# Kernel tuning notes

Hardware: AMD Instinct MI355X
Metric: run time of the kernel (lower is better)

Reference implementation:

```python
import jax, jax.numpy as jnp
import numpy as np
import math

B, S, HID, H = 1, 2048, 1024, 16
D = HID // H  # head_dim = 64


def setup_inputs() -> dict:
    key = jax.random.key(0)
    ks = jax.random.split(key, 12)
    s = 0.02
    x = jax.random.normal(ks[0], (B, S, HID), jnp.float32)
    Wq = jax.random.normal(ks[1], (HID, HID), jnp.float32) * s
    bq = jnp.zeros((HID,), jnp.float32)
    Wk = jax.random.normal(ks[2], (HID, HID), jnp.float32) * s
    bk = jnp.zeros((HID,), jnp.float32)
    Wv = jax.random.normal(ks[3], (HID, HID), jnp.float32) * s
    bv = jnp.zeros((HID,), jnp.float32)
    Wo = jax.random.normal(ks[4], (HID, HID), jnp.float32) * s
    bo = jnp.zeros((HID,), jnp.float32)
    # nn.Parameter(torch.ones(3,3)) at init; small noise so the bias is non-degenerate
    cmw = jnp.ones((3, 3), jnp.float32) + 0.1 * jax.random.normal(ks[5], (3, 3), jnp.float32)
    # full causal [B,S,S] mask so the mask.shape[1]==seq_len branch is taken
    mask = jnp.tril(jnp.ones((B, S, S), jnp.int32))
    modality_info = jax.random.randint(ks[6], (B, S), 0, 3, dtype=jnp.int64)
    return dict(x=x, Wq=Wq, bq=bq, Wk=Wk, bk=bk, Wv=Wv, bv=bv, Wo=Wo, bo=bo,
                cmw=cmw, mask=mask, modality_info=modality_info)


def reference(x, Wq, bq, Wk, bk, Wv, bv, Wo, bo, cmw, mask, modality_info):
    b, s, _ = x.shape
    # QKV projections (torch Linear: y = x @ W.T + b), split into heads [B,H,S,D]
    q = (x @ Wq.T + bq).reshape(b, s, H, D).transpose(0, 2, 1, 3)
    k = (x @ Wk.T + bk).reshape(b, s, H, D).transpose(0, 2, 1, 3)
    v = (x @ Wv.T + bv).reshape(b, s, H, D).transpose(0, 2, 1, 3)
    scores = jnp.einsum('bhqd,bhkd->bhqk', q, k) / math.sqrt(D)  # [B,H,S,S]
    # cross-modal bias: gather from 3x3 table via pairwise modality indices -> [B,S,S]
    bias = cmw[modality_info[:, :, None], modality_info[:, None, :]]
    scores = scores + bias[:, None, :, :]  # equals original broadcast when B==1
    scores = jnp.where(mask[:, None, :, :] == 0, -1e9, scores)
    attn = jax.nn.softmax(scores, axis=-1)  # dropout is identity in eval
    ctx = jnp.einsum('bhqk,bhkd->bhqd', attn, v)          # [B,H,S,D]
    ctx = ctx.transpose(0, 2, 1, 3).reshape(b, s, HID)    # [B,S,HID]
    return ctx @ Wo.T + bo
```

## Files before the change

kernel.cpp:

```cpp
#include <hip/hip_runtime.h>
#include <hip/hip_bf16.h>
#include <math.h>

#define S_LEN 2048
#define HID   1024
#define NHEAD 16

using bf16x8 = __attribute__((ext_vector_type(8))) short;
using bf16x4 = __attribute__((ext_vector_type(4))) short;
using f32x4  = __attribute__((ext_vector_type(4))) float;

__device__ __forceinline__ float bf2f(short s) {
  union { unsigned u; float f; } c;
  c.u = ((unsigned)(unsigned short)s) << 16;
  return c.f;
}
__device__ __forceinline__ short f2bf(float f) {
  union { float f; unsigned u; } c; c.f = f;
  unsigned u = c.u;
  unsigned r = (u + 0x7fffu + ((u >> 16) & 1u)) >> 16;
  return (short)r;
}
__device__ __forceinline__ float loadf(const void* base, long idx, int is_bf) {
  return is_bf ? bf2f(((const short*)base)[idx]) : ((const float*)base)[idx];
}
__device__ __forceinline__ void gl_lds16(const void* g, void* l) {
  __builtin_amdgcn_global_load_lds(
      (const __attribute__((address_space(1))) void*)g,
      (__attribute__((address_space(3))) void*)l, 16, 0, 0);
}

__global__ __launch_bounds__(256) void convert5(
    const void* __restrict__ s0, const void* __restrict__ s1, const void* __restrict__ s2,
    const void* __restrict__ s3, const void* __restrict__ s4,
    short* __restrict__ d0, short* __restrict__ d1, short* __restrict__ d2,
    short* __restrict__ d3, short* __restrict__ d4,
    const int* __restrict__ modw, int* __restrict__ flags) {
  __shared__ int sh_isbf;
  const int t = threadIdx.x;

  if (t < 64) {
    const unsigned* xw = (const unsigned*)s0;
    int cnt = 0;
    for (int i = t; i < 1024; i += 64) {
      const unsigned fld = (xw[i] >> 7) & 0xFFu;
      cnt += (fld >= 100u && fld <= 135u) ? 1 : 0;
    }
    for (int m = 1; m < 64; m <<= 1) cnt += __shfl_xor(cnt, m);
    if (t == 0) sh_isbf = (cnt >= 512) ? 1 : 0;
  }
  __syncthreads();
  const int is_bf = sh_isbf;

  if (blockIdx.x == 0 && blockIdx.y == 0 && t < 64) {
    int odd = 0;
    for (int i = 0; i < 4; ++i) {
      const int wv = modw[2 * (t + 64 * i) + 1];
      odd += (wv != 0) ? 1 : 0;
    }
    for (int m = 1; m < 64; m <<= 1) odd += __shfl_xor(odd, m);
    if (t == 0) {
      flags[0] = is_bf;
      flags[1] = (odd == 0) ? 1 : 0;
    }
  }

  const int a = blockIdx.y;
  const void* src = (a == 0) ? s0 : (a == 1) ? s1 : (a == 2) ? s2 : (a == 3) ? s3 : s4;
  short* dst = (a == 0) ? d0 : (a == 1) ? d1 : (a == 2) ? d2 : (a == 3) ? d3 : d4;
  const long n = (a == 0) ? (2L << 20) : (1L << 20);
  long i = (long)(blockIdx.x * 256 + t) * 8;
  const long stride = (long)gridDim.x * 256 * 8;
  if (is_bf) {
    for (; i < n; i += stride)
      *(bf16x8*)(dst + i) = *(const bf16x8*)((const short*)src + i);
  } else {
    for (; i < n; i += stride) {
      const float* p = (const float*)src + i;
      bf16x8 r;
#pragma unroll
      for (int j = 0; j < 8; ++j) r[j] = f2bf(p[j]);
      *(bf16x8*)(dst + i) = r;
    }
  }
}

template <int BM, int BN>
__global__ __launch_bounds__(256) void gemm_bt3(
    const short* __restrict__ A,
    const short* __restrict__ W0, const short* __restrict__ W1, const short* __restrict__ W2,
    const void* __restrict__ b0, const void* __restrict__ b1, const void* __restrict__ b2,
    void* __restrict__ C0, void* __restrict__ C1, void* __restrict__ C2,
    const int* __restrict__ flags, int nbn, int store_f32)
{
  constexpr int K = 1024;
  constexpr int N = 1024;
  constexpr int WM = (BM == 128) ? 2 : 1;
  constexpr int WN = 4 / WM;
  constexpr int MI = (BM / 16) / WM;
  constexpr int NI = (BN / 16) / WN;
  __shared__ short As[2][BM * 32];
  __shared__ short Bs[2][BN * 32];

  const int t = threadIdx.x;
  const int w = t >> 6, lane = t & 63;
  const int l15 = lane & 15, quad = lane >> 4;
  const int wm = w / WN, wn = w % WN;
  const int is_bf = flags[0];

  const int mat = blockIdx.x / nbn;
  const int n0 = (blockIdx.x % nbn) * BN;
  const int m0 = blockIdx.y * BM;

  const short* W  = (mat == 0) ? W0 : (mat == 1 ? W1 : W2);
  const void* bia = (mat == 0) ? b0 : (mat == 1 ? b1 : b2);
  void*       C   = (mat == 0) ? C0 : (mat == 1 ? C1 : C2);

  f32x4 acc[MI][NI];
  for (int mi = 0; mi < MI; ++mi)
    for (int ni = 0; ni < NI; ++ni)
      for (int r = 0; r < 4; ++r) acc[mi][ni][r] = 0.f;

  const int srow = t >> 2;
  const int sch  = (t & 3) * 8;
  const short* Ap = A + (long)(m0 + srow) * K + sch;
  const short* Wp = W + (long)(n0 + srow) * K + sch;

  auto stage = [&](int kt, int buf) {
    short* ad = &As[buf][w * 512];
    short* bd = &Bs[buf][w * 512];
    gl_lds16(Ap + kt * 32, ad);
    if (BM == 128) gl_lds16(Ap + kt * 32 + 64L * K, ad + 2048);
    gl_lds16(Wp + kt * 32, bd);
    if (BN == 128) gl_lds16(Wp + kt * 32 + 64L * K, bd + 2048);
  };

  stage(0, 0);
  int cur = 0;
  for (int kt = 0; kt < K / 32; ++kt) {
    __syncthreads();
    if (kt + 1 < K / 32) stage(kt + 1, cur ^ 1);

    bf16x8 af[MI], bfr[NI];
    for (int mi = 0; mi < MI; ++mi)
      af[mi] = *(const bf16x8*)&As[cur][(wm * (MI * 16) + mi * 16 + l15) * 32 + quad * 8];
    for (int ni = 0; ni < NI; ++ni)
      bfr[ni] = *(const bf16x8*)&Bs[cur][(wn * (NI * 16) + ni * 16 + l15) * 32 + quad * 8];
    for (int mi = 0; mi < MI; ++mi)
      for (int ni = 0; ni < NI; ++ni)
        acc[mi][ni] = __builtin_amdgcn_mfma_f32_16x16x32_bf16(af[mi], bfr[ni], acc[mi][ni], 0, 0, 0);
    cur ^= 1;
  }

  for (int ni = 0; ni < NI; ++ni) {
    const int col = n0 + wn * (NI * 16) + ni * 16 + l15;
    const float bv = loadf(bia, col, is_bf);
    for (int mi = 0; mi < MI; ++mi) {
      const int row = m0 + wm * (MI * 16) + mi * 16 + quad * 4;
      for (int r = 0; r < 4; ++r) {
        const float v = acc[mi][ni][r] + bv;
        const long idx = (long)(row + r) * N + col;
        if (store_f32) ((float*)C)[idx] = v;
        else           ((short*)C)[idx] = f2bf(v);
      }
    }
  }
}

__global__ __launch_bounds__(256) void attn_split(
    const short* __restrict__ Q, const short* __restrict__ Kg, const short* __restrict__ Vg,
    const int* __restrict__ mod, const void* __restrict__ cmw,
    const int* __restrict__ flags,
    short* __restrict__ PO0, short* __restrict__ PO1,
    float* __restrict__ PL)
{
  __shared__ short Ks[2][64 * 80];
  __shared__ short Vt[2][64 * 80];
  __shared__ short Ps[4 * 16 * 80];
  __shared__ float cm[9];
  __shared__ int mods[2048];

  const int t = threadIdx.x;
  const int w = t >> 6, lane = t & 63;
  const int l15 = lane & 15, quad = lane >> 4;
  const int h = blockIdx.y;
  const int pair = blockIdx.x >> 1;
  const int par  = blockIdx.x & 1;
  const int m64 = flags[1];
  const float KL2E = 0.125f * 1.44269504089f;

  if (t < 9) cm[t] = loadf(cmw, t, flags[0]) * 1.44269504089f;
  for (int i = t; i < 2048; i += 256) mods[i] = mod[i << m64];
  __syncthreads();

  short* POp = (par == 0) ? PO0 : PO1;
  const int krow = t >> 3, kch = (t & 7) * 8;
  const int vkp = t & 63, vdc = (t >> 6) * 8;

  for (int si = 0; si < 2; ++si) {
    const int strip = (si == 0) ? pair : 31 - pair;
    const int q0 = strip * 64;
    const int nkt = strip + 1;

    const short* qb = Q + (long)(q0 + w * 16 + l15) * HID + h * 64 + quad * 8;
    const bf16x8 aq0 = *(const bf16x8*)qb;
    const bf16x8 aq1 = *(const bf16x8*)(qb + 32);

    int mrow[4];
    for (int r = 0; r < 4; ++r) mrow[r] = mods[q0 + w * 16 + quad * 4 + r];

    float lsum[4];
    f32x4 acc_o[4];
    for (int r = 0; r < 4; ++r) lsum[r] = 0.f;
    for (int ni = 0; ni < 4; ++ni)
      for (int r = 0; r < 4; ++r) acc_o[ni][r] = 0.f;

    bf16x8 rk0, rk1, rv0, rv1;
    auto preload = [&](int kt) {
      const long kb = (long)(kt * 64) * HID + h * 64;
      rk0 = *(const bf16x8*)(Kg + kb + (long)krow * HID + kch);
      rk1 = *(const bf16x8*)(Kg + kb + (long)(krow + 32) * HID + kch);
      rv0 = *(const bf16x8*)(Vg + kb + (long)vkp * HID + vdc);
      rv1 = *(const bf16x8*)(Vg + kb + (long)vkp * HID + 32 + vdc);
    };
    auto writebuf = [&](int buf) {
      *(bf16x8*)&Ks[buf][krow * 80 + kch] = rk0;
      *(bf16x8*)&Ks[buf][(krow + 32) * 80 + kch] = rk1;
#pragma unroll
      for (int j = 0; j < 8; ++j) Vt[buf][(vdc + j) * 80 + vkp] = rv0[j];
#pragma unroll
      for (int j = 0; j < 8; ++j) Vt[buf][(vdc + 32 + j) * 80 + vkp] = rv1[j];
    };

    if (par < nkt) {
      __syncthreads();
      preload(par);
      writebuf(0);
      if (par + 2 < nkt) preload(par + 2);
    }

    int cur = 0;
    for (int kt = par; kt < nkt; kt += 2) {
      __syncthreads();

      f32x4 sc[4];
      __builtin_amdgcn_s_setprio(1);
      for (int nt = 0; nt < 4; ++nt) {
        const bf16x8 kb0 = *(const bf16x8*)&Ks[cur][(nt * 16 + l15) * 80 + quad * 8];
        const bf16x8 kb1 = *(const bf16x8*)&Ks[cur][(nt * 16 + l15) * 80 + 32 + quad * 8];
        f32x4 z;
        for (int r = 0; r < 4; ++r) z[r] = 0.f;
        z = __builtin_amdgcn_mfma_f32_16x16x32_bf16(aq0, kb0, z, 0, 0, 0);
        z = __builtin_amdgcn_mfma_f32_16x16x32_bf16(aq1, kb1, z, 0, 0, 0);
        sc[nt] = z;
      }
      __builtin_amdgcn_s_setprio(0);

      if (kt + 2 < nkt) {
        writebuf(cur ^ 1);
        if (kt + 4 < nkt) preload(kt + 4);
      }

      float sv[4][4];
      for (int nt = 0; nt < 4; ++nt) {
        const int mcol = mods[kt * 64 + nt * 16 + l15];
        for (int r = 0; r < 4; ++r)
          sv[nt][r] = sc[nt][r] * KL2E + cm[mrow[r] * 3 + mcol];
      }
      if (kt == nkt - 1) {
        for (int nt = 0; nt < 4; ++nt) {
          const int col = kt * 64 + nt * 16 + l15;
          for (int r = 0; r < 4; ++r) {
            const int row = q0 + w * 16 + quad * 4 + r;
            sv[nt][r] = (col <= row) ? sv[nt][r] : -1e30f;
          }
        }
      }
      short pb[4][4];
      for (int nt = 0; nt < 4; ++nt)
        for (int r = 0; r < 4; ++r) {
          const float p = __builtin_exp2f(fminf(sv[nt][r], 86.56f));
          lsum[r] += p;
          pb[nt][r] = f2bf(p);
        }

      short* Pw = &Ps[w * 16 * 80];
      for (int nt = 0; nt < 4; ++nt)
        for (int r = 0; r < 4; ++r)
          Pw[(quad * 4 + r) * 80 + nt * 16 + l15] = pb[nt][r];
      asm volatile("s_waitcnt lgkmcnt(0)" ::: "memory");

      __builtin_amdgcn_s_setprio(1);
      for (int kk = 0; kk < 2; ++kk) {
        const bf16x8 ap = *(const bf16x8*)&Pw[l15 * 80 + kk * 32 + quad * 8];
        for (int ni = 0; ni < 4; ++ni) {
          const bf16x8 bv = *(const bf16x8*)&Vt[cur][(ni * 16 + l15) * 80 + kk * 32 + quad * 8];
          acc_o[ni] = __builtin_amdgcn_mfma_f32_16x16x32_bf16(ap, bv, acc_o[ni], 0, 0, 0);
        }
      }
      __builtin_amdgcn_s_setprio(0);
      cur ^= 1;
    }

    for (int off = 1; off < 16; off <<= 1)
      for (int r = 0; r < 4; ++r) lsum[r] += __shfl_xor(lsum[r], off);

    for (int ni = 0; ni < 4; ++ni) {
      const int col = h * 64 + ni * 16 + l15;
      for (int r = 0; r < 4; ++r) {
        const int row = q0 + w * 16 + quad * 4 + r;
        POp[(long)row * HID + col] = f2bf(acc_o[ni][r]);
      }
    }
    if (l15 == 0) {
      for (int r = 0; r < 4; ++r) {
        const int row = q0 + w * 16 + quad * 4 + r;
        PL[par * 32768 + row * 16 + h] = lsum[r];
      }
    }
  }
}

__global__ __launch_bounds__(256) void attn_merge(
    const short* __restrict__ PO0, const short* __restrict__ PO1,
    const float* __restrict__ PL, short* __restrict__ CTX)
{
  const int row = blockIdx.x;
  const int t = threadIdx.x;
  const int h = t >> 4;
  const int d0 = (t & 15) * 4;
  const float l0 = PL[row * 16 + h], l1 = PL[32768 + row * 16 + h];
  const float inv = 1.f / (l0 + l1);
  const long b = (long)row * HID + h * 64 + d0;
  const bf16x4 o0 = *(const bf16x4*)&PO0[b];
  const bf16x4 o1 = *(const bf16x4*)&PO1[b];
  bf16x4 out;
#pragma unroll
  for (int j = 0; j < 4; ++j)
    out[j] = f2bf((bf2f(o0[j]) + bf2f(o1[j])) * inv);
  *(bf16x4*)&CTX[b] = out;
}

extern "C" void kernel_launch(void* const* d_in, const int* in_sizes, int n_in,
                              void* d_out, int out_size, void* d_ws, size_t ws_size,
                              hipStream_t stream) {
  constexpr long M1 = 1024L * 1024L;
  int*   flags = (int*)d_ws;
  short* base  = (short*)d_ws + 128;
  short* xb  = base;
  short* Wqb = xb + 2 * M1;
  short* Wkb = Wqb + M1;
  short* Wvb = Wkb + M1;
  short* Wob = Wvb + M1;
  short* Qw  = Wob + M1;
  short* Kw  = Qw + 2 * M1;
  short* Vw  = Kw + 2 * M1;
  short* CTX = Vw + 2 * M1;
  short* PO0 = CTX;
  short* PO1 = xb;
  float* PL  = (float*)Wvb;
  const int* modality = (const int*)d_in[11];

  convert5<<<dim3(512, 5), 256, 0, stream>>>(
      d_in[0], d_in[1], d_in[3], d_in[5], d_in[7],
      xb, Wqb, Wkb, Wvb, Wob, modality, flags);

  gemm_bt3<128, 64><<<dim3(48, 16), 256, 0, stream>>>(
      xb, Wqb, Wkb, Wvb, d_in[2], d_in[4], d_in[6],
      Qw, Kw, Vw, flags, 16, 0);
  attn_split<<<dim3(32, NHEAD), 256, 0, stream>>>(
      Qw, Kw, Vw, modality, d_in[9], flags, PO0, PO1, PL);
  attn_merge<<<dim3(S_LEN), 256, 0, stream>>>(PO0, PO1, PL, CTX);
  gemm_bt3<64, 64><<<dim3(16, 32), 256, 0, stream>>>(
      CTX, Wob, Wob, Wob, d_in[8], d_in[8], d_in[8],
      d_out, d_out, d_out, flags, 16, 1);
}
```

Measured before the change: 182.4 us.

## Rewrite attention with 32x32 MFMA, register-resident P, and 4-way KV split

```diff
diff --git a/kernel.cpp b/kernel.cpp
--- a/kernel.cpp
+++ b/kernel.cpp
@@ -9,6 +9,8 @@
 using bf16x8 = __attribute__((ext_vector_type(8))) short;
 using bf16x4 = __attribute__((ext_vector_type(4))) short;
 using f32x4  = __attribute__((ext_vector_type(4))) float;
+using f32x16 = __attribute__((ext_vector_type(16))) float;
+using i32x4  = __attribute__((ext_vector_type(4))) int;
 
 __device__ __forceinline__ float bf2f(short s) {
   union { unsigned u; float f; } c;
@@ -20,6 +22,11 @@
   unsigned u = c.u;
   unsigned r = (u + 0x7fffu + ((u >> 16) & 1u)) >> 16;
   return (short)r;
+}
+__device__ __forceinline__ unsigned cvtpk(float lo, float hi) {
+  unsigned r;
+  asm("v_cvt_pk_bf16_f32 %0, %1, %2" : "=v"(r) : "v"(lo), "v"(hi));
+  return r;
 }
 __device__ __forceinline__ float loadf(const void* base, long idx, int is_bf) {
   return is_bf ? bf2f(((const short*)base)[idx]) : ((const float*)base)[idx];
@@ -167,25 +174,24 @@
   }
 }
 
+#define POSTRIDE (2L * 1024 * 1024)
 __global__ __launch_bounds__(256) void attn_split(
     const short* __restrict__ Q, const short* __restrict__ Kg, const short* __restrict__ Vg,
     const int* __restrict__ mod, const void* __restrict__ cmw,
     const int* __restrict__ flags,
-    short* __restrict__ PO0, short* __restrict__ PO1,
-    float* __restrict__ PL)
+    short* __restrict__ PO, float* __restrict__ PL)
 {
-  __shared__ short Ks[2][64 * 80];
-  __shared__ short Vt[2][64 * 80];
-  __shared__ short Ps[4 * 16 * 80];
+  __shared__ short Ks[64 * 72];
+  __shared__ short Vt[64 * 72];
   __shared__ float cm[9];
   __shared__ int mods[2048];
 
   const int t = threadIdx.x;
   const int w = t >> 6, lane = t & 63;
-  const int l15 = lane & 15, quad = lane >> 4;
+  const int l31 = lane & 31, hi = lane >> 5;
   const int h = blockIdx.y;
-  const int pair = blockIdx.x >> 1;
-  const int par  = blockIdx.x & 1;
+  const int p   = blockIdx.x >> 2;
+  const int par = blockIdx.x & 3;
   const int m64 = flags[1];
   const float KL2E = 0.125f * 1.44269504089f;
 
@@ -193,151 +199,157 @@
   for (int i = t; i < 2048; i += 256) mods[i] = mod[i << m64];
   __syncthreads();
 
-  short* POp = (par == 0) ? PO0 : PO1;
+  short* POp = PO + (long)par * POSTRIDE;
+
   const int krow = t >> 3, kch = (t & 7) * 8;
-  const int vkp = t & 63, vdc = (t >> 6) * 8;
+  const int vk = (t & 31) * 2, vd = (t >> 5) * 8;
+
+  bf16x8 rk0, rk1, rv0, rv1;
+  auto preload = [&](int kt) {
+    const long kb = (long)(kt * 64) * HID + h * 64;
+    rk0 = *(const bf16x8*)(Kg + kb + (long)krow * HID + kch);
+    rk1 = *(const bf16x8*)(Kg + kb + (long)(krow + 32) * HID + kch);
+    rv0 = *(const bf16x8*)(Vg + kb + (long)vk * HID + vd);
+    rv1 = *(const bf16x8*)(Vg + kb + (long)(vk + 1) * HID + vd);
+  };
+  auto writebuf = [&]() {
+    *(bf16x8*)&Ks[krow * 72 + kch] = rk0;
+    *(bf16x8*)&Ks[(krow + 32) * 72 + kch] = rk1;
+#pragma unroll
+    for (int j = 0; j < 8; ++j) {
+      const unsigned pk = ((unsigned)(unsigned short)rv0[j]) |
+                          (((unsigned)(unsigned short)rv1[j]) << 16);
+      *(unsigned*)&Vt[(vd + j) * 72 + vk] = pk;
+    }
+  };
 
   for (int si = 0; si < 2; ++si) {
-    const int strip = (si == 0) ? pair : 31 - pair;
-    const int q0 = strip * 64;
-    const int nkt = strip + 1;
-
-    const short* qb = Q + (long)(q0 + w * 16 + l15) * HID + h * 64 + quad * 8;
-    const bf16x8 aq0 = *(const bf16x8*)qb;
-    const bf16x8 aq1 = *(const bf16x8*)(qb + 32);
-
-    int mrow[4];
-    for (int r = 0; r < 4; ++r) mrow[r] = mods[q0 + w * 16 + quad * 4 + r];
-
-    float lsum[4];
-    f32x4 acc_o[4];
-    for (int r = 0; r < 4; ++r) lsum[r] = 0.f;
-    for (int ni = 0; ni < 4; ++ni)
-      for (int r = 0; r < 4; ++r) acc_o[ni][r] = 0.f;
-
-    bf16x8 rk0, rk1, rv0, rv1;
-    auto preload = [&](int kt) {
-      const long kb = (long)(kt * 64) * HID + h * 64;
-      rk0 = *(const bf16x8*)(Kg + kb + (long)krow * HID + kch);
-      rk1 = *(const bf16x8*)(Kg + kb + (long)(krow + 32) * HID + kch);
-      rv0 = *(const bf16x8*)(Vg + kb + (long)vkp * HID + vdc);
-      rv1 = *(const bf16x8*)(Vg + kb + (long)vkp * HID + 32 + vdc);
-    };
-    auto writebuf = [&](int buf) {
-      *(bf16x8*)&Ks[buf][krow * 80 + kch] = rk0;
-      *(bf16x8*)&Ks[buf][(krow + 32) * 80 + kch] = rk1;
-#pragma unroll
-      for (int j = 0; j < 8; ++j) Vt[buf][(vdc + j) * 80 + vkp] = rv0[j];
-#pragma unroll
-      for (int j = 0; j < 8; ++j) Vt[buf][(vdc + 32 + j) * 80 + vkp] = rv1[j];
-    };
-
-    if (par < nkt) {
-      __syncthreads();
+    const int strip = si ? 15 - p : p;
+    const int q0 = strip * 128;
+    const int ktmax = 2 * strip + 1;
+    const int qg = q0 + w * 32 + l31;
+
+    const short* qptr = Q + (long)qg * HID + h * 64 + hi * 8;
+    bf16x8 qf[4];
+#pragma unroll
+    for (int ds = 0; ds < 4; ++ds) qf[ds] = *(const bf16x8*)(qptr + ds * 16);
+
+    const int mrow = mods[qg];
+    const float c0 = cm[mrow * 3], c1 = cm[mrow * 3 + 1], c2 = cm[mrow * 3 + 2];
+
+    float lsum = 0.f;
+    f32x16 acc0, acc1;
+#pragma unroll
+    for (int r = 0; r < 16; ++r) { acc0[r] = 0.f; acc1[r] = 0.f; }
+
+    if (par <= ktmax) {
       preload(par);
-      writebuf(0);
-      if (par + 2 < nkt) preload(par + 2);
-    }
-
-    int cur = 0;
-    for (int kt = par; kt < nkt; kt += 2) {
-      __syncthreads();
-
-      f32x4 sc[4];
-      __builtin_amdgcn_s_setprio(1);
-      for (int nt = 0; nt < 4; ++nt) {
-        const bf16x8 kb0 = *(const bf16x8*)&Ks[cur][(nt * 16 + l15) * 80 + quad * 8];
-        const bf16x8 kb1 = *(const bf16x8*)&Ks[cur][(nt * 16 + l15) * 80 + 32 + quad * 8];
-        f32x4 z;
-        for (int r = 0; r < 4; ++r) z[r] = 0.f;
-        z = __builtin_amdgcn_mfma_f32_16x16x32_bf16(aq0, kb0, z, 0, 0, 0);
-        z = __builtin_amdgcn_mfma_f32_16x16x32_bf16(aq1, kb1, z, 0, 0, 0);
-        sc[nt] = z;
-      }
-      __builtin_amdgcn_s_setprio(0);
-
-      if (kt + 2 < nkt) {
-        writebuf(cur ^ 1);
-        if (kt + 4 < nkt) preload(kt + 4);
-      }
-
-      float sv[4][4];
-      for (int nt = 0; nt < 4; ++nt) {
-        const int mcol = mods[kt * 64 + nt * 16 + l15];
-        for (int r = 0; r < 4; ++r)
-          sv[nt][r] = sc[nt][r] * KL2E + cm[mrow[r] * 3 + mcol];
-      }
-      if (kt == nkt - 1) {
-        for (int nt = 0; nt < 4; ++nt) {
-          const int col = kt * 64 + nt * 16 + l15;
-          for (int r = 0; r < 4; ++r) {
-            const int row = q0 + w * 16 + quad * 4 + r;
-            sv[nt][r] = (col <= row) ? sv[nt][r] : -1e30f;
+      for (int kt = par; kt <= ktmax; kt += 4) {
+        __syncthreads();
+        writebuf();
+        __syncthreads();
+        if (kt + 4 <= ktmax) preload(kt + 4);
+
+        f32x16 sc0, sc1;
+#pragma unroll
+        for (int r = 0; r < 16; ++r) { sc0[r] = 0.f; sc1[r] = 0.f; }
+#pragma unroll
+        for (int ds = 0; ds < 4; ++ds) {
+          const bf16x8 kf0 = *(const bf16x8*)&Ks[l31 * 72 + ds * 16 + hi * 8];
+          const bf16x8 kf1 = *(const bf16x8*)&Ks[(32 + l31) * 72 + ds * 16 + hi * 8];
+          sc0 = __builtin_amdgcn_mfma_f32_32x32x16_bf16(kf0, qf[ds], sc0, 0, 0, 0);
+          sc1 = __builtin_amdgcn_mfma_f32_32x32x16_bf16(kf1, qf[ds], sc1, 0, 0, 0);
+        }
+
+        const bool diag = (kt >= 2 * strip);
+        auto smax = [&](f32x16& S, int kh) {
+#pragma unroll
+          for (int g = 0; g < 4; ++g) {
+            const i32x4 mc = *(const i32x4*)&mods[kt * 64 + 32 * kh + 8 * g + 4 * hi];
+#pragma unroll
+            for (int i = 0; i < 4; ++i) {
+              const int r = 4 * g + i;
+              const int kgl = kt * 64 + 32 * kh + 8 * g + 4 * hi + i;
+              const int m = mc[i];
+              const float bias = (m == 0) ? c0 : ((m == 1) ? c1 : c2);
+              float sv = S[r] * KL2E + bias;
+              if (diag && kgl > qg) sv = -1e30f;
+              const float pe = __builtin_exp2f(fminf(sv, 86.56f));
+              lsum += pe;
+              S[r] = pe;
+            }
           }
+        };
+        smax(sc0, 0);
+        smax(sc1, 1);
+
+        bf16x8 pa[4];
+#pragma unroll
+        for (int ks = 0; ks < 4; ++ks) {
+          const f32x16& P = (ks < 2) ? sc0 : sc1;
+          const int rb = (ks & 1) * 8;
+          const unsigned A  = cvtpk(P[rb + 0], P[rb + 1]);
+          const unsigned B  = cvtpk(P[rb + 2], P[rb + 3]);
+          const unsigned Cc = cvtpk(P[rb + 4], P[rb + 5]);
+          const unsigned D  = cvtpk(P[rb + 6], P[rb + 7]);
+          const unsigned e1 = hi ? A : Cc;
+          const unsigned e2 = hi ? B : D;
+          const unsigned s1 = (unsigned)__shfl_xor((int)e1, 32);
+          const unsigned s2 = (unsigned)__shfl_xor((int)e2, 32);
+          union { unsigned u[4]; bf16x8 v; } fr;
+          fr.u[0] = hi ? s1 : A;
+          fr.u[1] = hi ? s2 : B;
+          fr.u[2] = hi ? Cc : s1;
+          fr.u[3] = hi ? D  : s2;
+          pa[ks] = fr.v;
+        }
+
+#pragma unroll
+        for (int ks = 0; ks < 4; ++ks) {
+          const bf16x8 vf0 = *(const bf16x8*)&Vt[l31 * 72 + ks * 16 + hi * 8];
+          const bf16x8 vf1 = *(const bf16x8*)&Vt[(32 + l31) * 72 + ks * 16 + hi * 8];
+          acc0 = __builtin_amdgcn_mfma_f32_32x32x16_bf16(pa[ks], vf0, acc0, 0, 0, 0);
+          acc1 = __builtin_amdgcn_mfma_f32_32x32x16_bf16(pa[ks], vf1, acc1, 0, 0, 0);
         }
       }
-      short pb[4][4];
-      for (int nt = 0; nt < 4; ++nt)
-        for (int r = 0; r < 4; ++r) {
-          const float p = __builtin_exp2f(fminf(sv[nt][r], 86.56f));
-          lsum[r] += p;
-          pb[nt][r] = f2bf(p);
-        }
-
-      short* Pw = &Ps[w * 16 * 80];
-      for (int nt = 0; nt < 4; ++nt)
-        for (int r = 0; r < 4; ++r)
-          Pw[(quad * 4 + r) * 80 + nt * 16 + l15] = pb[nt][r];
-      asm volatile("s_waitcnt lgkmcnt(0)" ::: "memory");
-
-      __builtin_amdgcn_s_setprio(1);
-      for (int kk = 0; kk < 2; ++kk) {
-        const bf16x8 ap = *(const bf16x8*)&Pw[l15 * 80 + kk * 32 + quad * 8];
-        for (int ni = 0; ni < 4; ++ni) {
-          const bf16x8 bv = *(const bf16x8*)&Vt[cur][(ni * 16 + l15) * 80 + kk * 32 + quad * 8];
-          acc_o[ni] = __builtin_amdgcn_mfma_f32_16x16x32_bf16(ap, bv, acc_o[ni], 0, 0, 0);
-        }
-      }
-      __builtin_amdgcn_s_setprio(0);
-      cur ^= 1;
-    }
-
-    for (int off = 1; off < 16; off <<= 1)
-      for (int r = 0; r < 4; ++r) lsum[r] += __shfl_xor(lsum[r], off);
-
-    for (int ni = 0; ni < 4; ++ni) {
-      const int col = h * 64 + ni * 16 + l15;
-      for (int r = 0; r < 4; ++r) {
-        const int row = q0 + w * 16 + quad * 4 + r;
-        POp[(long)row * HID + col] = f2bf(acc_o[ni][r]);
-      }
-    }
-    if (l15 == 0) {
-      for (int r = 0; r < 4; ++r) {
-        const int row = q0 + w * 16 + quad * 4 + r;
-        PL[par * 32768 + row * 16 + h] = lsum[r];
-      }
-    }
+    }
+
+    lsum += __shfl_xor(lsum, 32);
+
+#pragma unroll
+    for (int r = 0; r < 16; ++r) {
+      const int row = q0 + w * 32 + (r & 3) + 8 * (r >> 2) + 4 * hi;
+      POp[(long)row * HID + h * 64 + l31]      = f2bf(acc0[r]);
+      POp[(long)row * HID + h * 64 + 32 + l31] = f2bf(acc1[r]);
+    }
+    if (lane < 32)
+      PL[par * 32768 + (q0 + w * 32 + lane) * 16 + h] = lsum;
   }
 }
 
 __global__ __launch_bounds__(256) void attn_merge(
-    const short* __restrict__ PO0, const short* __restrict__ PO1,
-    const float* __restrict__ PL, short* __restrict__ CTX)
+    const short* __restrict__ PO, const float* __restrict__ PL,
+    short* __restrict__ CTX)
 {
   const int row = blockIdx.x;
   const int t = threadIdx.x;
   const int h = t >> 4;
   const int d0 = (t & 15) * 4;
-  const float l0 = PL[row * 16 + h], l1 = PL[32768 + row * 16 + h];
-  const float inv = 1.f / (l0 + l1);
+  float ls = 0.f;
+#pragma unroll
+  for (int i = 0; i < 4; ++i) ls += PL[i * 32768 + row * 16 + h];
+  const float inv = 1.f / ls;
   const long b = (long)row * HID + h * 64 + d0;
-  const bf16x4 o0 = *(const bf16x4*)&PO0[b];
-  const bf16x4 o1 = *(const bf16x4*)&PO1[b];
+  float o[4] = {0.f, 0.f, 0.f, 0.f};
+#pragma unroll
+  for (int i = 0; i < 4; ++i) {
+    const bf16x4 v = *(const bf16x4*)&PO[i * POSTRIDE + b];
+#pragma unroll
+    for (int j = 0; j < 4; ++j) o[j] += bf2f(v[j]);
+  }
   bf16x4 out;
 #pragma unroll
-  for (int j = 0; j < 4; ++j)
-    out[j] = f2bf((bf2f(o0[j]) + bf2f(o1[j])) * inv);
+  for (int j = 0; j < 4; ++j) out[j] = f2bf(o[j] * inv);
   *(bf16x4*)&CTX[b] = out;
 }
 
@@ -356,9 +368,8 @@
   short* Kw  = Qw + 2 * M1;
   short* Vw  = Kw + 2 * M1;
   short* CTX = Vw + 2 * M1;
-  short* PO0 = CTX;
-  short* PO1 = xb;
-  float* PL  = (float*)Wvb;
+  short* PO4 = base + 14 * M1;
+  float* PL4 = (float*)(base + 22 * M1);
   const int* modality = (const int*)d_in[11];
 
   convert5<<<dim3(512, 5), 256, 0, stream>>>(
@@ -369,8 +380,8 @@
       xb, Wqb, Wkb, Wvb, d_in[2], d_in[4], d_in[6],
       Qw, Kw, Vw, flags, 16, 0);
   attn_split<<<dim3(32, NHEAD), 256, 0, stream>>>(
-      Qw, Kw, Vw, modality, d_in[9], flags, PO0, PO1, PL);
-  attn_merge<<<dim3(S_LEN), 256, 0, stream>>>(PO0, PO1, PL, CTX);
+      Qw, Kw, Vw, modality, d_in[9], flags, PO4, PL4);
+  attn_merge<<<dim3(S_LEN), 256, 0, stream>>>(PO4, PL4, CTX);
   gemm_bt3<64, 64><<<dim3(16, 32), 256, 0, stream>>>(
       CTX, Wob, Wob, Wob, d_in[8], d_in[8], d_in[8],
       d_out, d_out, d_out, flags, 16, 1);
```

Measured after the change: 204.6 us. 12.1% more time.

## Split attention keys four ways with 128-row query strips and 512-thread blocks

Applied to the files above, without the earlier changes.

```diff
diff --git a/kernel.cpp b/kernel.cpp
--- a/kernel.cpp
+++ b/kernel.cpp
@@ -167,16 +167,16 @@
   }
 }
 
-__global__ __launch_bounds__(256) void attn_split(
+#define POSTRIDE (2L * 1024 * 1024)
+__global__ __launch_bounds__(512) void attn_split(
     const short* __restrict__ Q, const short* __restrict__ Kg, const short* __restrict__ Vg,
     const int* __restrict__ mod, const void* __restrict__ cmw,
     const int* __restrict__ flags,
-    short* __restrict__ PO0, short* __restrict__ PO1,
-    float* __restrict__ PL)
+    short* __restrict__ PO, float* __restrict__ PL)
 {
-  __shared__ short Ks[2][64 * 80];
-  __shared__ short Vt[2][64 * 80];
-  __shared__ short Ps[4 * 16 * 80];
+  __shared__ short Ks[64 * 80];
+  __shared__ short Vt[64 * 80];
+  __shared__ short Ps[8 * 16 * 80];
   __shared__ float cm[9];
   __shared__ int mods[2048];
 
@@ -184,30 +184,31 @@
   const int w = t >> 6, lane = t & 63;
   const int l15 = lane & 15, quad = lane >> 4;
   const int h = blockIdx.y;
-  const int pair = blockIdx.x >> 1;
-  const int par  = blockIdx.x & 1;
+  const int p   = blockIdx.x >> 2;
+  const int par = blockIdx.x & 3;
   const int m64 = flags[1];
   const float KL2E = 0.125f * 1.44269504089f;
 
   if (t < 9) cm[t] = loadf(cmw, t, flags[0]) * 1.44269504089f;
-  for (int i = t; i < 2048; i += 256) mods[i] = mod[i << m64];
+  for (int i = t; i < 2048; i += 512) mods[i] = mod[i << m64];
   __syncthreads();
 
-  short* POp = (par == 0) ? PO0 : PO1;
+  short* POp = PO + (long)par * POSTRIDE;
   const int krow = t >> 3, kch = (t & 7) * 8;
   const int vkp = t & 63, vdc = (t >> 6) * 8;
 
   for (int si = 0; si < 2; ++si) {
-    const int strip = (si == 0) ? pair : 31 - pair;
-    const int q0 = strip * 64;
-    const int nkt = strip + 1;
-
-    const short* qb = Q + (long)(q0 + w * 16 + l15) * HID + h * 64 + quad * 8;
+    const int strip = si ? 15 - p : p;
+    const int q0 = strip * 128;
+    const int ktmax = 2 * strip + 1;
+    const int qw0 = q0 + w * 16;
+
+    const short* qb = Q + (long)(qw0 + l15) * HID + h * 64 + quad * 8;
     const bf16x8 aq0 = *(const bf16x8*)qb;
     const bf16x8 aq1 = *(const bf16x8*)(qb + 32);
 
     int mrow[4];
-    for (int r = 0; r < 4; ++r) mrow[r] = mods[q0 + w * 16 + quad * 4 + r];
+    for (int r = 0; r < 4; ++r) mrow[r] = mods[qw0 + quad * 4 + r];
 
     float lsum[4];
     f32x4 acc_o[4];
@@ -215,91 +216,77 @@
     for (int ni = 0; ni < 4; ++ni)
       for (int r = 0; r < 4; ++r) acc_o[ni][r] = 0.f;
 
-    bf16x8 rk0, rk1, rv0, rv1;
+    bf16x8 rk, rv;
     auto preload = [&](int kt) {
       const long kb = (long)(kt * 64) * HID + h * 64;
-      rk0 = *(const bf16x8*)(Kg + kb + (long)krow * HID + kch);
-      rk1 = *(const bf16x8*)(Kg + kb + (long)(krow + 32) * HID + kch);
-      rv0 = *(const bf16x8*)(Vg + kb + (long)vkp * HID + vdc);
-      rv1 = *(const bf16x8*)(Vg + kb + (long)vkp * HID + 32 + vdc);
+      rk = *(const bf16x8*)(Kg + kb + (long)krow * HID + kch);
+      rv = *(const bf16x8*)(Vg + kb + (long)vkp * HID + vdc);
     };
-    auto writebuf = [&](int buf) {
-      *(bf16x8*)&Ks[buf][krow * 80 + kch] = rk0;
-      *(bf16x8*)&Ks[buf][(krow + 32) * 80 + kch] = rk1;
-#pragma unroll
-      for (int j = 0; j < 8; ++j) Vt[buf][(vdc + j) * 80 + vkp] = rv0[j];
-#pragma unroll
-      for (int j = 0; j < 8; ++j) Vt[buf][(vdc + 32 + j) * 80 + vkp] = rv1[j];
-    };
-
-    if (par < nkt) {
-      __syncthreads();
+
+    if (par <= ktmax) {
       preload(par);
-      writebuf(0);
-      if (par + 2 < nkt) preload(par + 2);
-    }
-
-    int cur = 0;
-    for (int kt = par; kt < nkt; kt += 2) {
-      __syncthreads();
-
-      f32x4 sc[4];
-      __builtin_amdgcn_s_setprio(1);
-      for (int nt = 0; nt < 4; ++nt) {
-        const bf16x8 kb0 = *(const bf16x8*)&Ks[cur][(nt * 16 + l15) * 80 + quad * 8];
-        const bf16x8 kb1 = *(const bf16x8*)&Ks[cur][(nt * 16 + l15) * 80 + 32 + quad * 8];
-        f32x4 z;
-        for (int r = 0; r < 4; ++r) z[r] = 0.f;
-        z = __builtin_amdgcn_mfma_f32_16x16x32_bf16(aq0, kb0, z, 0, 0, 0);
-        z = __builtin_amdgcn_mfma_f32_16x16x32_bf16(aq1, kb1, z, 0, 0, 0);
-        sc[nt] = z;
-      }
-      __builtin_amdgcn_s_setprio(0);
-
-      if (kt + 2 < nkt) {
-        writebuf(cur ^ 1);
-        if (kt + 4 < nkt) preload(kt + 4);
-      }
-
-      float sv[4][4];
-      for (int nt = 0; nt < 4; ++nt) {
-        const int mcol = mods[kt * 64 + nt * 16 + l15];
-        for (int r = 0; r < 4; ++r)
-          sv[nt][r] = sc[nt][r] * KL2E + cm[mrow[r] * 3 + mcol];
-      }
-      if (kt == nkt - 1) {
-        for (int nt = 0; nt < 4; ++nt) {
-          const int col = kt * 64 + nt * 16 + l15;
-          for (int r = 0; r < 4; ++r) {
-            const int row = q0 + w * 16 + quad * 4 + r;
-            sv[nt][r] = (col <= row) ? sv[nt][r] : -1e30f;
+      for (int kt = par; kt <= ktmax; kt += 4) {
+        __syncthreads();
+        *(bf16x8*)&Ks[krow * 80 + kch] = rk;
+#pragma unroll
+        for (int j = 0; j < 8; ++j) Vt[(vdc + j) * 80 + vkp] = rv[j];
+        __syncthreads();
+        if (kt + 4 <= ktmax) preload(kt + 4);
+
+        if (kt * 64 <= qw0 + 15) {
+          f32x4 sc[4];
+          __builtin_amdgcn_s_setprio(1);
+          for (int nt = 0; nt < 4; ++nt) {
+            const bf16x8 kb0 = *(const bf16x8*)&Ks[(nt * 16 + l15) * 80 + quad * 8];
+            const bf16x8 kb1 = *(const bf16x8*)&Ks[(nt * 16 + l15) * 80 + 32 + quad * 8];
+            f32x4 z;
+            for (int r = 0; r < 4; ++r) z[r] = 0.f;
+            z = __builtin_amdgcn_mfma_f32_16x16x32_bf16(aq0, kb0, z, 0, 0, 0);
+            z = __builtin_amdgcn_mfma_f32_16x16x32_bf16(aq1, kb1, z, 0, 0, 0);
+            sc[nt] = z;
           }
+          __builtin_amdgcn_s_setprio(0);
+
+          float sv[4][4];
+          for (int nt = 0; nt < 4; ++nt) {
+            const int mcol = mods[kt * 64 + nt * 16 + l15];
+            for (int r = 0; r < 4; ++r)
+              sv[nt][r] = sc[nt][r] * KL2E + cm[mrow[r] * 3 + mcol];
+          }
+          if (kt * 64 + 63 > qw0) {
+            for (int nt = 0; nt < 4; ++nt) {
+              const int col = kt * 64 + nt * 16 + l15;
+              for (int r = 0; r < 4; ++r) {
+                const int row = qw0 + quad * 4 + r;
+                sv[nt][r] = (col <= row) ? sv[nt][r] : -1e30f;
+              }
+            }
+          }
+          short pb[4][4];
+          for (int nt = 0; nt < 4; ++nt)
+            for (int r = 0; r < 4; ++r) {
+              const float pe = __builtin_exp2f(fminf(sv[nt][r], 86.56f));
+              lsum[r] += pe;
+              pb[nt][r] = f2bf(pe);
+            }
+
+          short* Pw = &Ps[w * 16 * 80];
+          for (int nt = 0; nt < 4; ++nt)
+            for (int r = 0; r < 4; ++r)
+              Pw[(quad * 4 + r) * 80 + nt * 16 + l15] = pb[nt][r];
+          asm volatile("s_waitcnt lgkmcnt(0)" ::: "memory");
+
+          __builtin_amdgcn_s_setprio(1);
+          for (int kk = 0; kk < 2; ++kk) {
+            const bf16x8 ap = *(const bf16x8*)&Pw[l15 * 80 + kk * 32 + quad * 8];
+            for (int ni = 0; ni < 4; ++ni) {
+              const bf16x8 bv = *(const bf16x8*)&Vt[(ni * 16 + l15) * 80 + kk * 32 + quad * 8];
+              acc_o[ni] = __builtin_amdgcn_mfma_f32_16x16x32_bf16(ap, bv, acc_o[ni], 0, 0, 0);
+            }
+          }
+          __builtin_amdgcn_s_setprio(0);
         }
       }
-      short pb[4][4];
-      for (int nt = 0; nt < 4; ++nt)
-        for (int r = 0; r < 4; ++r) {
-          const float p = __builtin_exp2f(fminf(sv[nt][r], 86.56f));
-          lsum[r] += p;
-          pb[nt][r] = f2bf(p);
-        }
-
-      short* Pw = &Ps[w * 16 * 80];
-      for (int nt = 0; nt < 4; ++nt)
-        for (int r = 0; r < 4; ++r)
-          Pw[(quad * 4 + r) * 80 + nt * 16 + l15] = pb[nt][r];
-      asm volatile("s_waitcnt lgkmcnt(0)" ::: "memory");
-
-      __builtin_amdgcn_s_setprio(1);
-      for (int kk = 0; kk < 2; ++kk) {
-        const bf16x8 ap = *(const bf16x8*)&Pw[l15 * 80 + kk * 32 + quad * 8];
-        for (int ni = 0; ni < 4; ++ni) {
-          const bf16x8 bv = *(const bf16x8*)&Vt[cur][(ni * 16 + l15) * 80 + kk * 32 + quad * 8];
-          acc_o[ni] = __builtin_amdgcn_mfma_f32_16x16x32_bf16(ap, bv, acc_o[ni], 0, 0, 0);
-        }
-      }
-      __builtin_amdgcn_s_setprio(0);
-      cur ^= 1;
     }
 
     for (int off = 1; off < 16; off <<= 1)
@@ -308,13 +295,13 @@
     for (int ni = 0; ni < 4; ++ni) {
       const int col = h * 64 + ni * 16 + l15;
       for (int r = 0; r < 4; ++r) {
-        const int row = q0 + w * 16 + quad * 4 + r;
+        const int row = qw0 + quad * 4 + r;
         POp[(long)row * HID + col] = f2bf(acc_o[ni][r]);
       }
     }
     if (l15 == 0) {
       for (int r = 0; r < 4; ++r) {
-        const int row = q0 + w * 16 + quad * 4 + r;
+        const int row = qw0 + quad * 4 + r;
         PL[par * 32768 + row * 16 + h] = lsum[r];
       }
     }
@@ -322,22 +309,28 @@
 }
 
 __global__ __launch_bounds__(256) void attn_merge(
-    const short* __restrict__ PO0, const short* __restrict__ PO1,
-    const float* __restrict__ PL, short* __restrict__ CTX)
+    const short* __restrict__ PO, const float* __restrict__ PL,
+    short* __restrict__ CTX)
 {
   const int row = blockIdx.x;
   const int t = threadIdx.x;
   const int h = t >> 4;
   const int d0 = (t & 15) * 4;
-  const float l0 = PL[row * 16 + h], l1 = PL[32768 + row * 16 + h];
-  const float inv = 1.f / (l0 + l1);
+  float ls = 0.f;
+#pragma unroll
+  for (int i = 0; i < 4; ++i) ls += PL[i * 32768 + row * 16 + h];
+  const float inv = 1.f / ls;
   const long b = (long)row * HID + h * 64 + d0;
-  const bf16x4 o0 = *(const bf16x4*)&PO0[b];
-  const bf16x4 o1 = *(const bf16x4*)&PO1[b];
+  float o[4] = {0.f, 0.f, 0.f, 0.f};
+#pragma unroll
+  for (int i = 0; i < 4; ++i) {
+    const bf16x4 v = *(const bf16x4*)&PO[i * POSTRIDE + b];
+#pragma unroll
+    for (int j = 0; j < 4; ++j) o[j] += bf2f(v[j]);
+  }
   bf16x4 out;
 #pragma unroll
-  for (int j = 0; j < 4; ++j)
-    out[j] = f2bf((bf2f(o0[j]) + bf2f(o1[j])) * inv);
+  for (int j = 0; j < 4; ++j) out[j] = f2bf(o[j] * inv);
   *(bf16x4*)&CTX[b] = out;
 }
 
@@ -356,9 +349,8 @@
   short* Kw  = Qw + 2 * M1;
   short* Vw  = Kw + 2 * M1;
   short* CTX = Vw + 2 * M1;
-  short* PO0 = CTX;
-  short* PO1 = xb;
-  float* PL  = (float*)Wvb;
+  short* PO4 = base + 14 * M1;
+  float* PL4 = (float*)(base + 22 * M1);
   const int* modality = (const int*)d_in[11];
 
   convert5<<<dim3(512, 5), 256, 0, stream>>>(
@@ -368,9 +360,9 @@
   gemm_bt3<128, 64><<<dim3(48, 16), 256, 0, stream>>>(
       xb, Wqb, Wkb, Wvb, d_in[2], d_in[4], d_in[6],
       Qw, Kw, Vw, flags, 16, 0);
-  attn_split<<<dim3(32, NHEAD), 256, 0, stream>>>(
-      Qw, Kw, Vw, modality, d_in[9], flags, PO0, PO1, PL);
-  attn_merge<<<dim3(S_LEN), 256, 0, stream>>>(PO0, PO1, PL, CTX);
+  attn_split<<<dim3(32, NHEAD), 512, 0, stream>>>(
+      Qw, Kw, Vw, modality, d_in[9], flags, PO4, PL4);
+  attn_merge<<<dim3(S_LEN), 256, 0, stream>>>(PO4, PL4, CTX);
   gemm_bt3<64, 64><<<dim3(16, 32), 256, 0, stream>>>(
       CTX, Wob, Wob, Wob, d_in[8], d_in[8], d_in[8],
       d_out, d_out, d_out, flags, 16, 1);
```

Result: faster. 178.6 us (-2.1%).
